# Performance work log

Hardware: AMD Instinct MI355X
Metric: run time of the kernel (lower is better)

The kernel has to match this reference:

```python
import jax, jax.numpy as jnp
import numpy as np

N, D_IN, D_OUT, NUM_GROUPS = 8192, 1024, 4096, 8


def setup_inputs() -> dict:
    key = jax.random.key(0)
    k_in, k_idx, k_w = jax.random.split(key, 3)
    inputs = jax.random.normal(k_in, (N, D_IN), dtype=jnp.float32)
    group_indices = jax.random.randint(k_idx, (N,), 0, NUM_GROUPS, dtype=jnp.int64)
    # VarianceScaling(1.0, fan_in) ~ stddev 1/sqrt(D_IN)
    w = jax.random.normal(k_w, (NUM_GROUPS, D_IN, D_OUT), dtype=jnp.float32) / np.sqrt(D_IN)
    b = jnp.zeros((NUM_GROUPS, D_OUT), dtype=jnp.float32)
    return {"inputs": inputs, "group_indices": group_indices, "w": w, "b": b}


def reference(inputs, group_indices, w, b):
    # Grouped GEMM: out[i] = inputs[i] @ w[g_i] + b[g_i].
    # Equivalent to the original gather -> per-group matmul -> inverse-permute
    # scatter, expressed jit-compatibly as masked dense GEMMs per group
    # (loop is over the small fixed expert count, not a data dim).
    num_groups = w.shape[0]
    out = jnp.zeros((inputs.shape[0], w.shape[-1]), dtype=inputs.dtype)
    for g in range(num_groups):
        mask = (group_indices == g)[:, None]  # [N, 1]
        masked_in = jnp.where(mask, inputs, 0)
        out = out + masked_in @ w[g] + jnp.where(mask, b[g], 0)
    return out
```

## Files before the change

### kernel.cpp

```cpp
#include <hip/hip_runtime.h>

#define N_ROWS 8192
#define D_IN 1024
#define D_OUT 4096
#define NGROUPS 8
#define NT_K 16
#define MAX_MT 72
#define NCONV 4096

typedef unsigned short ushort_t;
typedef __attribute__((ext_vector_type(8))) __bf16 bf16x8;
typedef __attribute__((ext_vector_type(4))) float f32x4;
typedef __attribute__((ext_vector_type(8))) unsigned short us8;

#define CTL_NT 28
#define CTL_TILES 32
#define CTL_SORTED 512

__device__ __forceinline__ unsigned short f2bf(float f) {
  union { float f; unsigned u; } v; v.f = f;
  unsigned r = v.u + 0x7FFFu + ((v.u >> 16) & 1u);
  return (unsigned short)(r >> 16);
}

__device__ __forceinline__ void gload_lds16(const void* g, void* l) {
  __builtin_amdgcn_global_load_lds(
      (const __attribute__((address_space(1))) void*)g,
      (__attribute__((address_space(3))) void*)l, 16, 0, 0);
}

__global__ __launch_bounds__(256) void k_prep(
    const float* __restrict__ A, const int* __restrict__ gi,
    const float* __restrict__ W, ushort_t* __restrict__ Ab,
    ushort_t* __restrict__ Wt, int* __restrict__ ctl,
    int* __restrict__ sorted) {
  __shared__ int hist[NGROUPS][256];
  __shared__ int base[NGROUPS];
  __shared__ float tile[64][66];
  const int bid = blockIdx.x;
  const int t = threadIdx.x;

  if (bid == 0) {
    int loc[NGROUPS];
#pragma unroll
    for (int gg = 0; gg < NGROUPS; ++gg) loc[gg] = 0;
    for (int i = 0; i < 32; ++i) ++loc[gi[t * 32 + i]];
#pragma unroll
    for (int gg = 0; gg < NGROUPS; ++gg) hist[gg][t] = loc[gg];
    __syncthreads();
    for (int d = 1; d < 256; d <<= 1) {
      int v[NGROUPS];
#pragma unroll
      for (int gg = 0; gg < NGROUPS; ++gg)
        v[gg] = (t >= d) ? hist[gg][t - d] : 0;
      __syncthreads();
#pragma unroll
      for (int gg = 0; gg < NGROUPS; ++gg) hist[gg][t] += v[gg];
      __syncthreads();
    }
    if (t == 0) {
      int off = 0, T = 0;
      int* tiles = ctl + CTL_TILES;
      for (int gg = 0; gg < NGROUPS; ++gg) {
        base[gg] = off;
        int c = hist[gg][255];
        for (int m0 = 0; m0 < c; m0 += 128) {
          tiles[T * 4 + 0] = gg;
          tiles[T * 4 + 1] = off + m0;
          tiles[T * 4 + 2] = min(128, c - m0);
          tiles[T * 4 + 3] = 0;
          ++T;
        }
        off += c;
      }
      ctl[CTL_NT] = T;
    }
    __syncthreads();
    int pos[NGROUPS];
#pragma unroll
    for (int gg = 0; gg < NGROUPS; ++gg)
      pos[gg] = base[gg] + hist[gg][t] - loc[gg];
    for (int i = 0; i < 32; ++i) {
      int g2 = gi[t * 32 + i];
      sorted[pos[g2]++] = t * 32 + i;
    }
  } else if (bid <= NCONV) {
    size_t i = ((size_t)(bid - 1) * 256 + t) * 8;
    float4 v0 = *reinterpret_cast<const float4*>(A + i);
    float4 v1 = *reinterpret_cast<const float4*>(A + i + 4);
    us8 o;
    o[0] = f2bf(v0.x); o[1] = f2bf(v0.y); o[2] = f2bf(v0.z); o[3] = f2bf(v0.w);
    o[4] = f2bf(v1.x); o[5] = f2bf(v1.y); o[6] = f2bf(v1.z); o[7] = f2bf(v1.w);
    *reinterpret_cast<us8*>(Ab + i) = o;
  } else {
    int idx = bid - 1 - NCONV;
    int g = idx >> 10;
    int rem = idx & 1023;
    int kt = rem >> 6;
    int n0 = (rem & 63) * 64;
    int k0 = kt * 64;
    int ln = (t & 15) * 4;
    int lk = t >> 4;
#pragma unroll
    for (int i = 0; i < 4; ++i) {
      int k = i * 16 + lk;
      float4 v = *reinterpret_cast<const float4*>(
          &W[((size_t)g * D_IN + k0 + k) * D_OUT + n0 + ln]);
      tile[k][ln] = v.x; tile[k][ln + 1] = v.y;
      tile[k][ln + 2] = v.z; tile[k][ln + 3] = v.w;
    }
    __syncthreads();
    int n = t & 63;
    int c0 = t >> 6;
#pragma unroll
    for (int i = 0; i < 2; ++i) {
      int c = c0 + i * 4;
      us8 u;
#pragma unroll
      for (int q = 0; q < 8; ++q) u[q] = f2bf(tile[c * 8 + q][n]);
      int slot = c ^ (n & 7);
      *reinterpret_cast<us8*>(
          &Wt[((size_t)(g * 16 + kt) * D_OUT + n0 + n) * 64 + slot * 8]) = u;
    }
  }
}


__global__ __launch_bounds__(256, 4) void k_gemm(
    const ushort_t* __restrict__ Ab, const ushort_t* __restrict__ Wt,
    const int* __restrict__ ctl, const int* __restrict__ sorted,
    const float* __restrict__ bias, float* __restrict__ out) {
  int bid = blockIdx.y * 32 + blockIdx.x;
  int xcd = bid & 7;
  int s = bid >> 3;
  int tI = (s >> 5) * 8 + xcd;
  int bx = s & 31;
  if (tI >= ctl[CTL_NT]) return;
  const int4 tl = reinterpret_cast<const int4*>(ctl + CTL_TILES)[tI];
  const int g = tl.x, start = tl.y, rows = tl.z;
  const int n_base = bx * 128;

  __shared__ ushort_t Asm[128 * 64];
  __shared__ ushort_t Bsm[128 * 64];
  __shared__ int rowid[128];

  const int t = threadIdx.x;
  const int lane = t & 63;
  const int w = t >> 6;
  if (t < 128) rowid[t] = sorted[start + ((t < rows) ? t : 0)];
  __syncthreads();

  const int lr = lane >> 3, lc = lane & 7;
  const int schunk = lc ^ lr;
  size_t aSrc[4];
  const ushort_t* bSrc[4];
  int ldOff[4];
  const ushort_t* bRegion = Wt + ((size_t)g * 16 * D_OUT + n_base) * 64;
#pragma unroll
  for (int j = 0; j < 4; ++j) {
    int I = j * 4 + w;
    aSrc[j] = (size_t)rowid[I * 8 + lr] * D_IN + schunk * 8;
    bSrc[j] = bRegion + I * 512 + lane * 8;
    ldOff[j] = I * 1024;
  }

  const int fr = lane & 15;
  const int fk = lane >> 4;
  const int fk16 = fk * 16;
  const int xr = (fr & 7) << 4;
  const int wm = (w >> 1) * 64;
  const int wn = (w & 1) * 64;
  const char* aCh = (const char*)Asm + (wm + fr) * 128;
  const char* bCh = (const char*)Bsm + (wn + fr) * 128;

  f32x4 acc[4][4];
#pragma unroll
  for (int a = 0; a < 4; ++a)
#pragma unroll
    for (int b = 0; b < 4; ++b) acc[a][b] = (f32x4){0.f, 0.f, 0.f, 0.f};

  bf16x8 Af[2][4], Bf[2][4];

  for (int kt = 0; kt < NT_K; ++kt) {
#pragma unroll
    for (int j = 0; j < 4; ++j)
      gload_lds16(Ab + aSrc[j] + (size_t)kt * 64, (char*)Asm + ldOff[j]);
#pragma unroll
    for (int j = 0; j < 4; ++j)
      gload_lds16(bSrc[j] + (size_t)kt * 262144, (char*)Bsm + ldOff[j]);
    __syncthreads();

#pragma unroll
    for (int ks = 0; ks < 2; ++ks) {
#pragma unroll
      for (int jm = 0; jm < 4; ++jm)
        Af[ks][jm] = *reinterpret_cast<const bf16x8*>(
            aCh + (jm * 16) * 128 + ((ks * 64 + fk16) ^ xr));
#pragma unroll
      for (int jn = 0; jn < 4; ++jn)
        Bf[ks][jn] = *reinterpret_cast<const bf16x8*>(
            bCh + (jn * 16) * 128 + ((ks * 64 + fk16) ^ xr));
    }
#pragma unroll
    for (int ks = 0; ks < 2; ++ks)
#pragma unroll
      for (int jm = 0; jm < 4; ++jm)
#pragma unroll
        for (int jn = 0; jn < 4; ++jn)
          acc[jm][jn] = __builtin_amdgcn_mfma_f32_16x16x32_bf16(
              Af[ks][jm], Bf[ks][jn], acc[jm][jn], 0, 0, 0);
    __syncthreads();
  }

  const float* bp = bias + g * D_OUT + n_base + wn;
  float bv[4];
#pragma unroll
  for (int nb = 0; nb < 4; ++nb) bv[nb] = bp[nb * 16 + fr];
#pragma unroll
  for (int mb = 0; mb < 4; ++mb) {
#pragma unroll
    for (int r = 0; r < 4; ++r) {
      int m = wm + mb * 16 + fk * 4 + r;
      if (m < rows) {
        size_t ro = (size_t)rowid[m] * D_OUT + n_base + wn;
#pragma unroll
        for (int nb = 0; nb < 4; ++nb)
          out[ro + nb * 16 + fr] = acc[mb][nb][r] + bv[nb];
      }
    }
  }
}

__global__ void k_naive(const float* __restrict__ A, const int* __restrict__ gi,
                        const float* __restrict__ W, const float* __restrict__ B,
                        float* __restrict__ out) {
  int row = blockIdx.x;
  int n = blockIdx.y * 256 + threadIdx.x;
  int g = gi[row];
  float s = B[(size_t)g * D_OUT + n];
  const float* wp = W + (size_t)g * D_IN * D_OUT + n;
  const float* a = A + (size_t)row * D_IN;
  for (int k = 0; k < D_IN; ++k) s += a[k] * wp[(size_t)k * D_OUT];
  out[(size_t)row * D_OUT + n] = s;
}

extern "C" void kernel_launch(void* const* d_in, const int* in_sizes, int n_in,
                              void* d_out, int out_size, void* d_ws, size_t ws_size,
                              hipStream_t stream) {
  const float* A = (const float*)d_in[0];
  const int* gi = (const int*)d_in[1];
  const float* W = (const float*)d_in[2];
  const float* B = (const float*)d_in[3];
  float* out = (float*)d_out;

  const size_t A_OFF = 65536;
  const size_t W_OFF = A_OFF + (size_t)N_ROWS * D_IN * 2;
  const size_t NEED = W_OFF + (size_t)NGROUPS * D_IN * D_OUT * 2;

  if (ws_size < NEED) {
    dim3 grid(N_ROWS, D_OUT / 256);
    k_naive<<<grid, dim3(256), 0, stream>>>(A, gi, W, B, out);
    return;
  }

  int* ctl = (int*)d_ws;
  int* sorted = ctl + CTL_SORTED;
  ushort_t* Ab = (ushort_t*)((char*)d_ws + A_OFF);
  ushort_t* Wt = (ushort_t*)((char*)d_ws + W_OFF);

  k_prep<<<1 + NCONV + 8192, 256, 0, stream>>>(A, gi, W, Ab, Wt, ctl, sorted);
  dim3 gg(32, MAX_MT);
  k_gemm<<<gg, 256, 0, stream>>>(Ab, Wt, ctl, sorted, B, out);
}
```

Before: 161.7 us.

## Switch grouped GEMM to 32x32x16 MFMA and remap block-to-XCD tile order

Replaces the 16x16x32 bf16 MFMA tiling (4x4 fragments per wave) with 32x32x16 MFMA (2x2 fragments), cutting LDS fragment reads per MFMA and using the larger instruction shape. It also changes how block IDs map to (tile, column) so that each XCD handles a fixed set of N-columns across all M tiles, aiming for better L2 reuse of the weight slices. Launch bounds occupancy drops from 4 to 3 blocks per SIMD group. The epilogue is rewritten for the 32x32 accumulator layout.

```diff
diff --git a/kernel.cpp b/kernel.cpp
--- a/kernel.cpp
+++ b/kernel.cpp
@@ -10,7 +10,7 @@
 
 typedef unsigned short ushort_t;
 typedef __attribute__((ext_vector_type(8))) __bf16 bf16x8;
-typedef __attribute__((ext_vector_type(4))) float f32x4;
+typedef __attribute__((ext_vector_type(16))) float f32x16;
 typedef __attribute__((ext_vector_type(8))) unsigned short us8;
 
 #define CTL_NT 28
@@ -126,15 +126,14 @@
 }
 
 
-__global__ __launch_bounds__(256, 4) void k_gemm(
+__global__ __launch_bounds__(256, 3) void k_gemm(
     const ushort_t* __restrict__ Ab, const ushort_t* __restrict__ Wt,
     const int* __restrict__ ctl, const int* __restrict__ sorted,
     const float* __restrict__ bias, float* __restrict__ out) {
   int bid = blockIdx.y * 32 + blockIdx.x;
-  int xcd = bid & 7;
-  int s = bid >> 3;
-  int tI = (s >> 5) * 8 + xcd;
-  int bx = s & 31;
+  int hi = bid >> 3;
+  int tI = hi % MAX_MT;
+  int bx = (bid & 7) * 4 + hi / MAX_MT;
   if (tI >= ctl[CTL_NT]) return;
   const int4 tl = reinterpret_cast<const int4*>(ctl + CTL_TILES)[tI];
   const int g = tl.x, start = tl.y, rows = tl.z;
@@ -164,22 +163,21 @@
     ldOff[j] = I * 1024;
   }
 
-  const int fr = lane & 15;
-  const int fk = lane >> 4;
-  const int fk16 = fk * 16;
-  const int xr = (fr & 7) << 4;
+  const int cr = lane & 31;
+  const int kh = lane >> 5;
+  const int xr = (cr & 7) << 4;
   const int wm = (w >> 1) * 64;
   const int wn = (w & 1) * 64;
-  const char* aCh = (const char*)Asm + (wm + fr) * 128;
-  const char* bCh = (const char*)Bsm + (wn + fr) * 128;
-
-  f32x4 acc[4][4];
-#pragma unroll
-  for (int a = 0; a < 4; ++a)
-#pragma unroll
-    for (int b = 0; b < 4; ++b) acc[a][b] = (f32x4){0.f, 0.f, 0.f, 0.f};
-
-  bf16x8 Af[2][4], Bf[2][4];
+  const char* aCh = (const char*)Asm + (wm + cr) * 128;
+  const char* bCh = (const char*)Bsm + (wn + cr) * 128;
+
+  f32x16 acc[2][2];
+#pragma unroll
+  for (int a = 0; a < 2; ++a)
+#pragma unroll
+    for (int b = 0; b < 2; ++b)
+#pragma unroll
+      for (int q = 0; q < 16; ++q) acc[a][b][q] = 0.f;
 
   for (int kt = 0; kt < NT_K; ++kt) {
 #pragma unroll
@@ -191,41 +189,39 @@
     __syncthreads();
 
 #pragma unroll
-    for (int ks = 0; ks < 2; ++ks) {
-#pragma unroll
-      for (int jm = 0; jm < 4; ++jm)
-        Af[ks][jm] = *reinterpret_cast<const bf16x8*>(
-            aCh + (jm * 16) * 128 + ((ks * 64 + fk16) ^ xr));
-#pragma unroll
-      for (int jn = 0; jn < 4; ++jn)
-        Bf[ks][jn] = *reinterpret_cast<const bf16x8*>(
-            bCh + (jn * 16) * 128 + ((ks * 64 + fk16) ^ xr));
-    }
-#pragma unroll
-    for (int ks = 0; ks < 2; ++ks)
-#pragma unroll
-      for (int jm = 0; jm < 4; ++jm)
-#pragma unroll
-        for (int jn = 0; jn < 4; ++jn)
-          acc[jm][jn] = __builtin_amdgcn_mfma_f32_16x16x32_bf16(
-              Af[ks][jm], Bf[ks][jn], acc[jm][jn], 0, 0, 0);
-    __syncthreads();
-  }
-
-  const float* bp = bias + g * D_OUT + n_base + wn;
-  float bv[4];
-#pragma unroll
-  for (int nb = 0; nb < 4; ++nb) bv[nb] = bp[nb * 16 + fr];
-#pragma unroll
-  for (int mb = 0; mb < 4; ++mb) {
-#pragma unroll
-    for (int r = 0; r < 4; ++r) {
-      int m = wm + mb * 16 + fk * 4 + r;
+    for (int ks = 0; ks < 4; ++ks) {
+      const int kb = ((ks * 32 + kh * 16) ^ xr);
+      bf16x8 Af[2], Bf[2];
+#pragma unroll
+      for (int mb = 0; mb < 2; ++mb)
+        Af[mb] = *reinterpret_cast<const bf16x8*>(aCh + mb * 32 * 128 + kb);
+#pragma unroll
+      for (int nb = 0; nb < 2; ++nb)
+        Bf[nb] = *reinterpret_cast<const bf16x8*>(bCh + nb * 32 * 128 + kb);
+#pragma unroll
+      for (int mb = 0; mb < 2; ++mb)
+#pragma unroll
+        for (int nb = 0; nb < 2; ++nb)
+          acc[mb][nb] = __builtin_amdgcn_mfma_f32_32x32x16_bf16(
+              Af[mb], Bf[nb], acc[mb][nb], 0, 0, 0);
+    }
+    __syncthreads();
+  }
+
+  float bv[2];
+#pragma unroll
+  for (int nb = 0; nb < 2; ++nb)
+    bv[nb] = bias[g * D_OUT + n_base + wn + nb * 32 + cr];
+#pragma unroll
+  for (int mb = 0; mb < 2; ++mb) {
+#pragma unroll
+    for (int q = 0; q < 16; ++q) {
+      int m = wm + mb * 32 + (q & 3) + 8 * (q >> 2) + 4 * kh;
       if (m < rows) {
-        size_t ro = (size_t)rowid[m] * D_OUT + n_base + wn;
-#pragma unroll
-        for (int nb = 0; nb < 4; ++nb)
-          out[ro + nb * 16 + fr] = acc[mb][nb][r] + bv[nb];
+        size_t ro = (size_t)rowid[m] * D_OUT + n_base + wn + cr;
+#pragma unroll
+        for (int nb = 0; nb < 2; ++nb)
+          out[ro + nb * 32] = acc[mb][nb][q] + bv[nb];
       }
     }
   }
```

New measurement: 166.7 us. +3.1%, slower.
